# Performance work log

Hardware: AMD Instinct MI355X
Metric: run time of the kernel (lower is better)

The kernel has to match this reference:

```python
import jax, jax.numpy as jnp
import numpy as np

C = 512
HEADS = 8
B, H, W = 2, 64, 64


def setup_inputs() -> dict:
    key = jax.random.key(0)
    k1, k2, k3, k4, k5 = jax.random.split(key, 5)
    s = 1.0 / np.sqrt(C)
    return {
        "hidden_states": jax.random.normal(k1, (B, C, H, W), dtype=jnp.float32),
        "qkv_w": jax.random.normal(k2, (3 * C, C), dtype=jnp.float32) * s,
        "qkv_b": jax.random.normal(k3, (3 * C,), dtype=jnp.float32) * 0.02,
        "proj_w": jax.random.normal(k4, (C, C), dtype=jnp.float32) * s,
        "proj_b": jax.random.normal(k5, (C,), dtype=jnp.float32) * 0.02,
    }


def reference(hidden_states, qkv_w, qkv_b, proj_w, proj_b):
    b, c, h, w = hidden_states.shape
    n = h * w  # sequence length
    heads = HEADS
    dim_head = c // heads
    scale = dim_head ** -0.5

    x = hidden_states.reshape(b, c, n)  # [b, c, n]
    # 1x1 conv1d == matmul over channel dim
    qkv = jnp.einsum("oc,bcn->bon", qkv_w, x) + qkv_b[None, :, None]  # [b, 3c, n]
    q, k, v = jnp.split(qkv, 3, axis=1)
    # [b, heads, dim_head, n] -> [b, heads, n, dim_head]
    def split_heads(t):
        return t.reshape(b, heads, dim_head, n).transpose(0, 1, 3, 2)
    q, k, v = split_heads(q), split_heads(k), split_heads(v)

    attn = jnp.einsum("bhqd,bhkd->bhqk", q, k) * scale  # [b, heads, n, n]
    attn = jax.nn.softmax(attn, axis=-1)
    out = jnp.einsum("bhqk,bhkd->bhqd", attn, v)  # [b, heads, n, dim_head]
    out = out.transpose(0, 1, 3, 2).reshape(b, c, n)  # [b, c, n]
    out = jnp.einsum("oc,bcn->bon", proj_w, out) + proj_b[None, :, None]
    return out  # [b, c, h*w] (matches torch module, no reshape back)
```

## Files before the change

### kernel.cpp

```cpp
#include <hip/hip_runtime.h>


typedef __attribute__((ext_vector_type(8))) short s16x8;
typedef __attribute__((ext_vector_type(4))) float f32x4;
typedef __attribute__((ext_vector_type(4))) unsigned short u16x4;

__device__ __forceinline__ unsigned short f2bf(float f) {
  unsigned u = __builtin_bit_cast(unsigned, f);
  u += 0x7fffu + ((u >> 16) & 1u);
  return (unsigned short)(u >> 16);
}

__device__ __forceinline__ unsigned cvt_pk_bf16(float lo, float hi) {
  unsigned r;
  asm("v_cvt_pk_bf16_f32 %0, %1, %2" : "=v"(r) : "v"(lo), "v"(hi));
  return r;
}

__global__ __launch_bounds__(256) void prep_weights(
    const float* __restrict__ qkv_w, const float* __restrict__ proj_w,
    short* __restrict__ wq, short* __restrict__ wp) {
  int t = blockIdx.x * 256 + threadIdx.x;
  const int NQ = 1536 * 512 / 4;
  if (t < NQ) {
    float4 v = ((const float4*)qkv_w)[t];
    u16x4 o; o[0] = f2bf(v.x); o[1] = f2bf(v.y); o[2] = f2bf(v.z); o[3] = f2bf(v.w);
    ((u16x4*)wq)[t] = o;
  } else {
    int t2 = t - NQ;
    float4 v = ((const float4*)proj_w)[t2];
    u16x4 o; o[0] = f2bf(v.x); o[1] = f2bf(v.y); o[2] = f2bf(v.z); o[3] = f2bf(v.w);
    ((u16x4*)wp)[t2] = o;
  }
}

__global__ __launch_bounds__(256) void prep_transpose(
    const float* __restrict__ x, short* __restrict__ xt) {
  __shared__ short TL[64 * 72];
  const int b = blockIdx.z, c0 = blockIdx.y * 64, n0 = blockIdx.x * 64;
  const int t = threadIdx.x;
  const int cr = t >> 4, n4 = (t & 15) * 4;
#pragma unroll
  for (int i = 0; i < 4; i++) {
    int c = cr + i * 16;
    float4 v = *(const float4*)(x + ((size_t)(b * 512 + c0 + c)) * 4096 + n0 + n4);
    TL[(n4 + 0) * 72 + c] = (short)f2bf(v.x);
    TL[(n4 + 1) * 72 + c] = (short)f2bf(v.y);
    TL[(n4 + 2) * 72 + c] = (short)f2bf(v.z);
    TL[(n4 + 3) * 72 + c] = (short)f2bf(v.w);
  }
  __syncthreads();
  const int n = t >> 2;
#pragma unroll
  for (int s2 = 0; s2 < 2; s2++) {
    int s = (t & 3) * 2 + s2;
    s16x8 v = *(const s16x8*)&TL[n * 72 + s * 8];
    *(s16x8*)(xt + ((size_t)(b * 4096 + n0 + n)) * 512 + c0 + s * 8) = v;
  }
}

__global__ __launch_bounds__(256) void qkv_gemm(
    const short* __restrict__ wq, const short* __restrict__ xt,
    const float* __restrict__ qkv_b,
    short* __restrict__ qkbuf,
    short* __restrict__ vbuf) {
  __shared__ short Al[128 * 40];
  __shared__ short Bl[128 * 40];
  const int b = blockIdx.z;
  const int m0 = blockIdx.y * 128, n0 = blockIdx.x * 128;
  const bool swapped = (blockIdx.y < 8);
  const int t = threadIdx.x, lane = t & 63, wid = t >> 6;
  const int wr = wid >> 1, wc = wid & 1;
  const int srow = t >> 1, scol = (t & 1) * 16;
  const short* gA = wq + (size_t)(m0 + srow) * 512 + scol;
  const short* gB = xt + ((size_t)(b * 4096 + n0 + srow)) * 512 + scol;
  short* lA = &Al[srow * 40 + scol];
  short* lB = &Bl[srow * 40 + scol];
  const short* As = swapped ? Bl : Al;
  const short* Bs = swapped ? Al : Bl;
  f32x4 acc[4][4] = {};
  for (int ks = 0; ks < 16; ks++) {
    *(s16x8*)lA       = *(const s16x8*)(gA + ks * 32);
    *(s16x8*)(lA + 8) = *(const s16x8*)(gA + ks * 32 + 8);
    *(s16x8*)lB       = *(const s16x8*)(gB + ks * 32);
    *(s16x8*)(lB + 8) = *(const s16x8*)(gB + ks * 32 + 8);
    __syncthreads();
    s16x8 af[4], bf[4];
#pragma unroll
    for (int i = 0; i < 4; i++) {
      af[i] = *(const s16x8*)&As[(wr * 64 + i * 16 + (lane & 15)) * 40 + ((lane >> 4) << 3)];
      bf[i] = *(const s16x8*)&Bs[(wc * 64 + i * 16 + (lane & 15)) * 40 + ((lane >> 4) << 3)];
    }
#pragma unroll
    for (int i = 0; i < 4; i++)
#pragma unroll
      for (int j = 0; j < 4; j++)
        acc[i][j] = __builtin_amdgcn_mfma_f32_16x16x32_bf16(af[i], bf[j], acc[i][j], 0, 0, 0);
    __syncthreads();
  }
  if (!swapped) {
#pragma unroll
    for (int i = 0; i < 4; i++)
#pragma unroll
      for (int r = 0; r < 4; r++) {
        int orow = m0 + wr * 64 + i * 16 + ((lane >> 4) << 2) + r;
        float bias = qkv_b[orow];
#pragma unroll
        for (int j = 0; j < 4; j++) {
          int ncol = n0 + wc * 64 + j * 16 + (lane & 15);
          vbuf[((size_t)(b * 512 + orow - 1024)) * 4096 + ncol] = (short)f2bf(acc[i][j][r] + bias);
        }
      }
  } else {
    const float qs = (m0 < 512) ? 0.18033688f : 1.0f;
#pragma unroll
    for (int j = 0; j < 4; j++) {
      int ocol = m0 + wc * 64 + j * 16 + (lane & 15);
      float bias = qkv_b[ocol];
#pragma unroll
      for (int i = 0; i < 4; i++)
#pragma unroll
        for (int r = 0; r < 4; r++) {
          int nrow = n0 + wr * 64 + i * 16 + ((lane >> 4) << 2) + r;
          qkbuf[((size_t)(b * 4096 + nrow)) * 1024 + ocol] = (short)f2bf((acc[i][j][r] + bias) * qs);
        }
    }
  }
}

__global__ __launch_bounds__(256) void flash_attn(
    const short* __restrict__ qkbuf, const short* __restrict__ vbuf,
    short* __restrict__ aout) {
  __shared__ short Kl[64 * 72];
  __shared__ short Vl[64 * 72];
  __shared__ short Pl[4 * 32 * 72];
  const int t = threadIdx.x, lane = t & 63, wid = t >> 6;
  const int g = lane >> 4, c = lane & 15;
  const int bh = blockIdx.y, b = bh >> 3, h = bh & 7;
  const int qbase = blockIdx.x * 128 + wid * 32;

  s16x8 qf[2][2];
#pragma unroll
  for (int mi = 0; mi < 2; mi++)
#pragma unroll
    for (int kd = 0; kd < 2; kd++)
      qf[mi][kd] = *(const s16x8*)(qkbuf + ((size_t)(b * 4096 + qbase + mi * 16 + c)) * 1024
                                   + h * 64 + kd * 32 + g * 8);

  f32x4 oacc[2][4] = {};
  float mrow[2] = {-__builtin_inff(), -__builtin_inff()};
  float lrow[2] = {0.f, 0.f};

  const int srow = t >> 2, sseg = (t & 3) * 16;
  const short* gK = qkbuf + ((size_t)(b * 4096 + srow)) * 1024 + 512 + h * 64 + sseg;
  const short* gV = vbuf + ((size_t)(b * 512 + h * 64 + srow)) * 4096 + sseg;
  short* lK = &Kl[srow * 72 + sseg];
  short* lV = &Vl[srow * 72 + sseg];
  short* myP = &Pl[wid * 32 * 72];

  s16x8 rK0 = *(const s16x8*)gK,       rK1 = *(const s16x8*)(gK + 8);
  s16x8 rV0 = *(const s16x8*)gV,       rV1 = *(const s16x8*)(gV + 8);

  for (int kt = 0; kt < 64; kt++) {
    *(s16x8*)lK = rK0;  *(s16x8*)(lK + 8) = rK1;
    *(s16x8*)lV = rV0;  *(s16x8*)(lV + 8) = rV1;
    __syncthreads();
    if (kt < 63) {
      const short* nK = gK + (size_t)(kt + 1) * 64 * 1024;
      const short* nV = gV + (kt + 1) * 64;
      rK0 = *(const s16x8*)nK;  rK1 = *(const s16x8*)(nK + 8);
      rV0 = *(const s16x8*)nV;  rV1 = *(const s16x8*)(nV + 8);
    }
    s16x8 kf[4][2];
#pragma unroll
    for (int ni = 0; ni < 4; ni++)
#pragma unroll
      for (int kd = 0; kd < 2; kd++)
        kf[ni][kd] = *(const s16x8*)&Kl[(ni * 16 + c) * 72 + kd * 32 + g * 8];
    f32x4 st[4][2] = {};
#pragma unroll
    for (int ni = 0; ni < 4; ni++)
#pragma unroll
      for (int mi = 0; mi < 2; mi++) {
        st[ni][mi] = __builtin_amdgcn_mfma_f32_16x16x32_bf16(kf[ni][0], qf[mi][0], st[ni][mi], 0, 0, 0);
        st[ni][mi] = __builtin_amdgcn_mfma_f32_16x16x32_bf16(kf[ni][1], qf[mi][1], st[ni][mi], 0, 0, 0);
      }
#pragma unroll
    for (int mi = 0; mi < 2; mi++) {
      float t01 = fmaxf(fmaxf(st[0][mi][0], st[0][mi][1]), fmaxf(st[0][mi][2], st[0][mi][3]));
      float t23 = fmaxf(fmaxf(st[1][mi][0], st[1][mi][1]), fmaxf(st[1][mi][2], st[1][mi][3]));
      float t45 = fmaxf(fmaxf(st[2][mi][0], st[2][mi][1]), fmaxf(st[2][mi][2], st[2][mi][3]));
      float t67 = fmaxf(fmaxf(st[3][mi][0], st[3][mi][1]), fmaxf(st[3][mi][2], st[3][mi][3]));
      float tm = fmaxf(fmaxf(t01, t23), fmaxf(t45, t67));
      tm = fmaxf(tm, __shfl_xor(tm, 16));
      tm = fmaxf(tm, __shfl_xor(tm, 32));
      float mn = fmaxf(mrow[mi], tm);
      float alpha = exp2f(mrow[mi] - mn);
      mrow[mi] = mn;
      float ps = 0.f;
#pragma unroll
      for (int ni = 0; ni < 4; ni++) {
        float p0 = exp2f(st[ni][mi][0] - mn);
        float p1 = exp2f(st[ni][mi][1] - mn);
        float p2 = exp2f(st[ni][mi][2] - mn);
        float p3 = exp2f(st[ni][mi][3] - mn);
        ps += (p0 + p1) + (p2 + p3);
        uint2 w;
        w.x = cvt_pk_bf16(p0, p1);
        w.y = cvt_pk_bf16(p2, p3);
        *(uint2*)&myP[(mi * 16 + c) * 72 + ni * 16 + g * 4] = w;
      }
      lrow[mi] = lrow[mi] * alpha + ps;
      float ar[4];
#pragma unroll
      for (int r = 0; r < 4; r++) ar[r] = __shfl(alpha, 20 * g + r);
#pragma unroll
      for (int di = 0; di < 4; di++)
#pragma unroll
        for (int r = 0; r < 4; r++) oacc[mi][di][r] *= ar[r];
    }
#pragma unroll
    for (int ks = 0; ks < 2; ks++) {
      s16x8 pa[2], vbf[4];
#pragma unroll
      for (int mi = 0; mi < 2; mi++)
        pa[mi] = *(const s16x8*)&myP[(mi * 16 + c) * 72 + ks * 32 + g * 8];
#pragma unroll
      for (int di = 0; di < 4; di++)
        vbf[di] = *(const s16x8*)&Vl[(di * 16 + c) * 72 + ks * 32 + g * 8];
#pragma unroll
      for (int mi = 0; mi < 2; mi++)
#pragma unroll
        for (int di = 0; di < 4; di++)
          oacc[mi][di] = __builtin_amdgcn_mfma_f32_16x16x32_bf16(pa[mi], vbf[di], oacc[mi][di], 0, 0, 0);
    }
    __syncthreads();
  }
#pragma unroll
  for (int mi = 0; mi < 2; mi++) {
    float l = lrow[mi];
    l += __shfl_xor(l, 16);
    l += __shfl_xor(l, 32);
    float inv = 1.f / l;
    float ir[4];
#pragma unroll
    for (int r = 0; r < 4; r++) ir[r] = __shfl(inv, 20 * g + r);
#pragma unroll
    for (int r = 0; r < 4; r++) {
      int qrow = qbase + mi * 16 + g * 4 + r;
#pragma unroll
      for (int di = 0; di < 4; di++) {
        int dc = di * 16 + c;
        aout[((size_t)(b * 4096 + qrow)) * 512 + h * 64 + dc] = (short)f2bf(oacc[mi][di][r] * ir[r]);
      }
    }
  }
}

__global__ __launch_bounds__(256) void proj_gemm(
    const short* __restrict__ wp, const short* __restrict__ aout,
    const float* __restrict__ proj_b, float* __restrict__ out) {
  __shared__ short Al[128 * 40];
  __shared__ short Bl[128 * 40];
  const int b = blockIdx.z;
  const int m0 = blockIdx.y * 128, n0 = blockIdx.x * 128;
  const int t = threadIdx.x, lane = t & 63, wid = t >> 6;
  const int wr = wid >> 1, wc = wid & 1;
  const int srow = t >> 1, scol = (t & 1) * 16;
  const short* gA = wp + (size_t)(m0 + srow) * 512 + scol;
  const short* gB = aout + ((size_t)(b * 4096 + n0 + srow)) * 512 + scol;
  short* lA = &Al[srow * 40 + scol];
  short* lB = &Bl[srow * 40 + scol];
  f32x4 acc[4][4] = {};
  for (int ks = 0; ks < 16; ks++) {
    *(s16x8*)lA       = *(const s16x8*)(gA + ks * 32);
    *(s16x8*)(lA + 8) = *(const s16x8*)(gA + ks * 32 + 8);
    *(s16x8*)lB       = *(const s16x8*)(gB + ks * 32);
    *(s16x8*)(lB + 8) = *(const s16x8*)(gB + ks * 32 + 8);
    __syncthreads();
    s16x8 af[4], bf[4];
#pragma unroll
    for (int i = 0; i < 4; i++) {
      af[i] = *(const s16x8*)&Al[(wr * 64 + i * 16 + (lane & 15)) * 40 + ((lane >> 4) << 3)];
      bf[i] = *(const s16x8*)&Bl[(wc * 64 + i * 16 + (lane & 15)) * 40 + ((lane >> 4) << 3)];
    }
#pragma unroll
    for (int i = 0; i < 4; i++)
#pragma unroll
      for (int j = 0; j < 4; j++)
        acc[i][j] = __builtin_amdgcn_mfma_f32_16x16x32_bf16(af[i], bf[j], acc[i][j], 0, 0, 0);
    __syncthreads();
  }
#pragma unroll
  for (int i = 0; i < 4; i++)
#pragma unroll
    for (int r = 0; r < 4; r++) {
      int orow = m0 + wr * 64 + i * 16 + ((lane >> 4) << 2) + r;
      float bias = proj_b[orow];
#pragma unroll
      for (int j = 0; j < 4; j++) {
        int ncol = n0 + wc * 64 + j * 16 + (lane & 15);
        out[((size_t)(b * 512 + orow)) * 4096 + ncol] = acc[i][j][r] + bias;
      }
    }
}

extern "C" void kernel_launch(void* const* d_in, const int* in_sizes, int n_in,
                              void* d_out, int out_size, void* d_ws, size_t ws_size,
                              hipStream_t stream) {
  const float* x      = (const float*)d_in[0];
  const float* qkv_w  = (const float*)d_in[1];
  const float* qkv_b  = (const float*)d_in[2];
  const float* proj_w = (const float*)d_in[3];
  const float* proj_b = (const float*)d_in[4];
  float* out = (float*)d_out;
  char* ws = (char*)d_ws;
  short* wq = (short*)(ws);
  short* wp = (short*)(ws + 1572864);
  short* xt = (short*)(ws + 2097152);
  short* qk = (short*)(ws + 10485760);
  short* vb = (short*)(ws + 27262976);
  short* ao = (short*)(ws + 35651584);

  prep_weights  <<<1024, 256, 0, stream>>>(qkv_w, proj_w, wq, wp);
  prep_transpose<<<dim3(64, 8, 2), 256, 0, stream>>>(x, xt);
  qkv_gemm      <<<dim3(32, 12, 2), 256, 0, stream>>>(wq, xt, qkv_b, qk, vb);
  flash_attn    <<<dim3(32, 16), 256, 0, stream>>>(qk, vb, ao);
  proj_gemm     <<<dim3(32, 4, 2), 256, 0, stream>>>(wp, ao, proj_b, out);
}
```

Baseline: 288.6 us.

## Split flash attention into 8 waves of 16 query rows with lazy rescale

The attention block now uses 512 threads, and each wave owns 16 query rows instead of 32. This halves per-wave MFMA work and register state and doubles the number of waves hiding latency per block. The output MFMA swaps operands so each lane's accumulator belongs to a single query row, which removes the alpha shuffles. Rescaling of the running max is skipped unless the new tile max exceeds the old one by more than 8 in log2 space. Each block still loads the same K/V tiles, so K/V LDS reuse per wave drops and there are more barrier participants.

```diff
diff --git a/kernel.cpp b/kernel.cpp
--- a/kernel.cpp
+++ b/kernel.cpp
@@ -128,48 +128,44 @@
   }
 }
 
-__global__ __launch_bounds__(256) void flash_attn(
+__global__ __launch_bounds__(512) void flash_attn(
     const short* __restrict__ qkbuf, const short* __restrict__ vbuf,
     short* __restrict__ aout) {
   __shared__ short Kl[64 * 72];
   __shared__ short Vl[64 * 72];
-  __shared__ short Pl[4 * 32 * 72];
+  __shared__ short Pl[8 * 16 * 72];
   const int t = threadIdx.x, lane = t & 63, wid = t >> 6;
   const int g = lane >> 4, c = lane & 15;
   const int bh = blockIdx.y, b = bh >> 3, h = bh & 7;
-  const int qbase = blockIdx.x * 128 + wid * 32;
-
-  s16x8 qf[2][2];
-#pragma unroll
-  for (int mi = 0; mi < 2; mi++)
-#pragma unroll
-    for (int kd = 0; kd < 2; kd++)
-      qf[mi][kd] = *(const s16x8*)(qkbuf + ((size_t)(b * 4096 + qbase + mi * 16 + c)) * 1024
-                                   + h * 64 + kd * 32 + g * 8);
-
-  f32x4 oacc[2][4] = {};
-  float mrow[2] = {-__builtin_inff(), -__builtin_inff()};
-  float lrow[2] = {0.f, 0.f};
-
-  const int srow = t >> 2, sseg = (t & 3) * 16;
+  const int qrow = blockIdx.x * 128 + wid * 16 + c;
+
+  s16x8 qf[2];
+#pragma unroll
+  for (int kd = 0; kd < 2; kd++)
+    qf[kd] = *(const s16x8*)(qkbuf + ((size_t)(b * 4096 + qrow)) * 1024
+                             + h * 64 + kd * 32 + g * 8);
+
+  f32x4 oacc[4] = {};
+  float m = -__builtin_inff();
+  float l = 0.f;
+
+  const int srow = t >> 3, sseg = (t & 7) * 8;
   const short* gK = qkbuf + ((size_t)(b * 4096 + srow)) * 1024 + 512 + h * 64 + sseg;
   const short* gV = vbuf + ((size_t)(b * 512 + h * 64 + srow)) * 4096 + sseg;
   short* lK = &Kl[srow * 72 + sseg];
   short* lV = &Vl[srow * 72 + sseg];
-  short* myP = &Pl[wid * 32 * 72];
-
-  s16x8 rK0 = *(const s16x8*)gK,       rK1 = *(const s16x8*)(gK + 8);
-  s16x8 rV0 = *(const s16x8*)gV,       rV1 = *(const s16x8*)(gV + 8);
+  short* myP = &Pl[wid * 16 * 72];
+
+  s16x8 rK = *(const s16x8*)gK;
+  s16x8 rV = *(const s16x8*)gV;
 
   for (int kt = 0; kt < 64; kt++) {
-    *(s16x8*)lK = rK0;  *(s16x8*)(lK + 8) = rK1;
-    *(s16x8*)lV = rV0;  *(s16x8*)(lV + 8) = rV1;
+    *(s16x8*)lK = rK;
+    *(s16x8*)lV = rV;
     __syncthreads();
     if (kt < 63) {
-      const short* nK = gK + (size_t)(kt + 1) * 64 * 1024;
-      const short* nV = gV + (kt + 1) * 64;
-      rK0 = *(const s16x8*)nK;  rK1 = *(const s16x8*)(nK + 8);
-      rV0 = *(const s16x8*)nV;  rV1 = *(const s16x8*)(nV + 8);
+      rK = *(const s16x8*)(gK + (size_t)(kt + 1) * 64 * 1024);
+      rV = *(const s16x8*)(gV + (kt + 1) * 64);
     }
     s16x8 kf[4][2];
 #pragma unroll
@@ -177,84 +173,67 @@
 #pragma unroll
       for (int kd = 0; kd < 2; kd++)
         kf[ni][kd] = *(const s16x8*)&Kl[(ni * 16 + c) * 72 + kd * 32 + g * 8];
-    f32x4 st[4][2] = {};
-#pragma unroll
-    for (int ni = 0; ni < 4; ni++)
-#pragma unroll
-      for (int mi = 0; mi < 2; mi++) {
-        st[ni][mi] = __builtin_amdgcn_mfma_f32_16x16x32_bf16(kf[ni][0], qf[mi][0], st[ni][mi], 0, 0, 0);
-        st[ni][mi] = __builtin_amdgcn_mfma_f32_16x16x32_bf16(kf[ni][1], qf[mi][1], st[ni][mi], 0, 0, 0);
-      }
-#pragma unroll
-    for (int mi = 0; mi < 2; mi++) {
-      float t01 = fmaxf(fmaxf(st[0][mi][0], st[0][mi][1]), fmaxf(st[0][mi][2], st[0][mi][3]));
-      float t23 = fmaxf(fmaxf(st[1][mi][0], st[1][mi][1]), fmaxf(st[1][mi][2], st[1][mi][3]));
-      float t45 = fmaxf(fmaxf(st[2][mi][0], st[2][mi][1]), fmaxf(st[2][mi][2], st[2][mi][3]));
-      float t67 = fmaxf(fmaxf(st[3][mi][0], st[3][mi][1]), fmaxf(st[3][mi][2], st[3][mi][3]));
-      float tm = fmaxf(fmaxf(t01, t23), fmaxf(t45, t67));
-      tm = fmaxf(tm, __shfl_xor(tm, 16));
-      tm = fmaxf(tm, __shfl_xor(tm, 32));
-      float mn = fmaxf(mrow[mi], tm);
-      float alpha = exp2f(mrow[mi] - mn);
-      mrow[mi] = mn;
-      float ps = 0.f;
-#pragma unroll
-      for (int ni = 0; ni < 4; ni++) {
-        float p0 = exp2f(st[ni][mi][0] - mn);
-        float p1 = exp2f(st[ni][mi][1] - mn);
-        float p2 = exp2f(st[ni][mi][2] - mn);
-        float p3 = exp2f(st[ni][mi][3] - mn);
-        ps += (p0 + p1) + (p2 + p3);
-        uint2 w;
-        w.x = cvt_pk_bf16(p0, p1);
-        w.y = cvt_pk_bf16(p2, p3);
-        *(uint2*)&myP[(mi * 16 + c) * 72 + ni * 16 + g * 4] = w;
-      }
-      lrow[mi] = lrow[mi] * alpha + ps;
-      float ar[4];
-#pragma unroll
-      for (int r = 0; r < 4; r++) ar[r] = __shfl(alpha, 20 * g + r);
+    f32x4 st[4] = {};
+#pragma unroll
+    for (int ni = 0; ni < 4; ni++) {
+      st[ni] = __builtin_amdgcn_mfma_f32_16x16x32_bf16(kf[ni][0], qf[0], st[ni], 0, 0, 0);
+      st[ni] = __builtin_amdgcn_mfma_f32_16x16x32_bf16(kf[ni][1], qf[1], st[ni], 0, 0, 0);
+    }
+    float t01 = fmaxf(fmaxf(st[0][0], st[0][1]), fmaxf(st[0][2], st[0][3]));
+    float t23 = fmaxf(fmaxf(st[1][0], st[1][1]), fmaxf(st[1][2], st[1][3]));
+    float t45 = fmaxf(fmaxf(st[2][0], st[2][1]), fmaxf(st[2][2], st[2][3]));
+    float t67 = fmaxf(fmaxf(st[3][0], st[3][1]), fmaxf(st[3][2], st[3][3]));
+    float tm = fmaxf(fmaxf(t01, t23), fmaxf(t45, t67));
+    tm = fmaxf(tm, __shfl_xor(tm, 16));
+    tm = fmaxf(tm, __shfl_xor(tm, 32));
+    if (!__all(tm <= m + 8.f)) {
+      float mn = fmaxf(m, tm);
+      float alpha = exp2f(m - mn);
+      m = mn;
+      l *= alpha;
 #pragma unroll
       for (int di = 0; di < 4; di++)
 #pragma unroll
-        for (int r = 0; r < 4; r++) oacc[mi][di][r] *= ar[r];
-    }
+        for (int r = 0; r < 4; r++) oacc[di][r] *= alpha;
+    }
+    float ps = 0.f;
+#pragma unroll
+    for (int ni = 0; ni < 4; ni++) {
+      float p0 = exp2f(st[ni][0] - m);
+      float p1 = exp2f(st[ni][1] - m);
+      float p2 = exp2f(st[ni][2] - m);
+      float p3 = exp2f(st[ni][3] - m);
+      ps += (p0 + p1) + (p2 + p3);
+      uint2 w;
+      w.x = cvt_pk_bf16(p0, p1);
+      w.y = cvt_pk_bf16(p2, p3);
+      *(uint2*)&myP[c * 72 + ni * 16 + g * 4] = w;
+    }
+    l += ps;
 #pragma unroll
     for (int ks = 0; ks < 2; ks++) {
-      s16x8 pa[2], vbf[4];
-#pragma unroll
-      for (int mi = 0; mi < 2; mi++)
-        pa[mi] = *(const s16x8*)&myP[(mi * 16 + c) * 72 + ks * 32 + g * 8];
+      s16x8 pa = *(const s16x8*)&myP[c * 72 + ks * 32 + g * 8];
+      s16x8 vbf[4];
 #pragma unroll
       for (int di = 0; di < 4; di++)
         vbf[di] = *(const s16x8*)&Vl[(di * 16 + c) * 72 + ks * 32 + g * 8];
 #pragma unroll
-      for (int mi = 0; mi < 2; mi++)
-#pragma unroll
-        for (int di = 0; di < 4; di++)
-          oacc[mi][di] = __builtin_amdgcn_mfma_f32_16x16x32_bf16(pa[mi], vbf[di], oacc[mi][di], 0, 0, 0);
-    }
-    __syncthreads();
-  }
-#pragma unroll
-  for (int mi = 0; mi < 2; mi++) {
-    float l = lrow[mi];
-    l += __shfl_xor(l, 16);
-    l += __shfl_xor(l, 32);
-    float inv = 1.f / l;
-    float ir[4];
-#pragma unroll
-    for (int r = 0; r < 4; r++) ir[r] = __shfl(inv, 20 * g + r);
+      for (int di = 0; di < 4; di++)
+        oacc[di] = __builtin_amdgcn_mfma_f32_16x16x32_bf16(vbf[di], pa, oacc[di], 0, 0, 0);
+    }
+    __syncthreads();
+  }
+  float lf = l;
+  lf += __shfl_xor(lf, 16);
+  lf += __shfl_xor(lf, 32);
+  float inv = 1.f / lf;
+#pragma unroll
+  for (int di = 0; di < 4; di++)
 #pragma unroll
     for (int r = 0; r < 4; r++) {
-      int qrow = qbase + mi * 16 + g * 4 + r;
-#pragma unroll
-      for (int di = 0; di < 4; di++) {
-        int dc = di * 16 + c;
-        aout[((size_t)(b * 4096 + qrow)) * 512 + h * 64 + dc] = (short)f2bf(oacc[mi][di][r] * ir[r]);
-      }
-    }
-  }
+      int d = di * 16 + g * 4 + r;
+      aout[((size_t)(b * 4096 + qrow)) * 512 + h * 64 + d] = (short)f2bf(oacc[di][r] * inv);
+    }
 }
 
 __global__ __launch_bounds__(256) void proj_gemm(
@@ -325,6 +304,6 @@
   prep_weights  <<<1024, 256, 0, stream>>>(qkv_w, proj_w, wq, wp);
   prep_transpose<<<dim3(64, 8, 2), 256, 0, stream>>>(x, xt);
   qkv_gemm      <<<dim3(32, 12, 2), 256, 0, stream>>>(wq, xt, qkv_b, qk, vb);
-  flash_attn    <<<dim3(32, 16), 256, 0, stream>>>(qk, vb, ao);
+  flash_attn    <<<dim3(32, 16), 512, 0, stream>>>(qk, vb, ao);
   proj_gemm     <<<dim3(32, 4, 2), 256, 0, stream>>>(wp, ao, proj_b, out);
 }
```

Result: faster. 253.8 us (-12.1%).
